# Kernel tuning notes

Measured on AMD Instinct MI355X. Metric: run time of the kernel, lower is better.

The kernel has to match this reference:

```python
import jax, jax.numpy as jnp
import numpy as np

RNN = 512        # rnn_units == embedding_units (required by LSTMCell input size)
ATT = 512        # attention_units
FEAT = 512       # feat_chans
VOCAB = 110
V1 = VOCAB + 1
MAX_LEN = 30
STEPS = MAX_LEN + 1
B, H, W = 32, 8, 32


def _lstm_cell(x, h, c, wih, whh, bih, bhh):
    # torch.nn.LSTMCell gate order: i, f, g, o
    gates = x @ wih.T + bih + h @ whh.T + bhh
    i, f, g, o = jnp.split(gates, 4, axis=-1)
    i, f, o = jax.nn.sigmoid(i), jax.nn.sigmoid(f), jax.nn.sigmoid(o)
    g = jnp.tanh(g)
    c_new = f * c + i * g
    h_new = o * jnp.tanh(c_new)
    return h_new, c_new


def setup_inputs() -> dict:
    key = jax.random.key(0)
    ks = jax.random.split(key, 16)
    s = 0.05

    def rn(k, shape):
        return jax.random.normal(k, shape, jnp.float32) * s

    return {
        "features": jax.random.normal(ks[0], (B, FEAT, H, W), jnp.float32),
        "holistic": jax.random.normal(ks[1], (B, RNN), jnp.float32),  # unused by forward (matches torch)
        "gt": jax.random.randint(ks[2], (B, STEPS), 0, V1),
        # AttentionModule params
        "W_feat": rn(ks[3], (ATT, FEAT, 3, 3)),
        "b_feat": jnp.zeros((ATT,), jnp.float32),
        "W_state": rn(ks[4], (ATT, RNN)),     # 1x1 conv, no bias
        "w_att": rn(ks[5], (ATT,)),           # 1x1 conv -> 1 channel, no bias
        # embedding (Linear, no bias): (embedding_units, vocab+1)
        "W_embed": rn(ks[6], (RNN, V1)),
        # LSTM cell 0
        "wih0": rn(ks[7], (4 * RNN, RNN)),
        "whh0": rn(ks[8], (4 * RNN, RNN)),
        "bih0": jnp.zeros((4 * RNN,), jnp.float32),
        "bhh0": jnp.zeros((4 * RNN,), jnp.float32),
        # LSTM cell 1
        "wih1": rn(ks[9], (4 * RNN, RNN)),
        "whh1": rn(ks[10], (4 * RNN, RNN)),
        "bih1": jnp.zeros((4 * RNN,), jnp.float32),
        "bhh1": jnp.zeros((4 * RNN,), jnp.float32),
        # output dense: (vocab+1, 2*rnn_units)
        "W_out": rn(ks[11], (V1, 2 * RNN)),
        "b_out": jnp.zeros((V1,), jnp.float32),
    }


def reference(features, holistic, gt, W_feat, b_feat, W_state, w_att, W_embed,
              wih0, whh0, bih0, bhh0, wih1, whh1, bih1, bhh1, W_out, b_out):
    Bsz, C, Hh, Ww = features.shape
    dt = features.dtype

    # feat_conv(features) is invariant across decode steps -> compute once
    feat_proj = jax.lax.conv_general_dilated(
        features, W_feat, window_strides=(1, 1), padding="SAME",
        dimension_numbers=("NCHW", "OIHW", "NCHW"),
    ) + b_feat[None, :, None, None]  # (B, ATT, H, W)

    # teacher-forced symbols: step 0 uses zeros, step t uses one_hot(gt[:, t-1])
    syms = jnp.concatenate(
        [jnp.zeros((Bsz, 1, V1), dt), jax.nn.one_hot(gt[:, :STEPS - 1], V1, dtype=dt)],
        axis=1,
    )
    syms = jnp.swapaxes(syms, 0, 1)  # (STEPS, B, V1)

    z = jnp.zeros((Bsz, RNN), dt)
    init = (z, z, z, z)  # h0, c0, h1, c1 (torch LSTMCell defaults to zero state)

    def step(carry, sym):
        h0, c0, h1, c1 = carry
        x = sym @ W_embed.T                                  # (B, RNN)
        h0, c0 = _lstm_cell(x, h0, c0, wih0, whh0, bih0, bhh0)
        h1, c1 = _lstm_cell(h0, h1, c1, wih1, whh1, bih1, bhh1)
        # attention glimpse: state is h1 broadcast as a 1x1 feature map
        sp = h1 @ W_state.T                                  # (B, ATT)
        proj = jnp.tanh(feat_proj + sp[:, :, None, None])    # (B, ATT, H, W)
        att = jnp.einsum("bahw,a->bhw", proj, w_att).reshape(Bsz, -1)
        att = jax.nn.softmax(att, axis=1).reshape(Bsz, Hh, Ww)
        glimpse = jnp.einsum("bchw,bhw->bc", features, att)  # (B, FEAT)
        logits = jnp.concatenate([h1, glimpse], axis=1) @ W_out.T + b_out
        return (h0, c0, h1, c1), logits

    _, logits = jax.lax.scan(step, init, syms)               # (STEPS, B, V1)
    return jnp.swapaxes(logits, 0, 1)                        # (B, STEPS, V1)
```

## Files before the change

### kernel.cpp

```cpp
#include <hip/hip_runtime.h>
#include <hip/hip_bf16.h>


#define RNN   512
#define V1    111
#define STEPS 31
#define HWP   256
#define POOLF 11008
#define NWG   128

typedef unsigned short ushortT;
typedef unsigned int   uintT;
typedef __attribute__((ext_vector_type(8))) short bf16x8;
typedef __attribute__((ext_vector_type(4))) float f32x4;

__device__ __forceinline__ float blo(uintT u){ union { uintT i; float f; } v; v.i = u << 16; return v.f; }
__device__ __forceinline__ float bhi(uintT u){ union { uintT i; float f; } v; v.i = u & 0xffff0000u; return v.f; }
__device__ __forceinline__ ushortT f2b(float f){
  __hip_bfloat16 h = __float2bfloat16(f);
  union { __hip_bfloat16 b; ushortT s; } v; v.b = h; return v.s;
}
__device__ __forceinline__ uintT packbf(float lo, float hi){
  return (uintT)f2b(lo) | ((uintT)f2b(hi) << 16);
}
__device__ __forceinline__ bf16x8 u4_to_b8(uint4 u){
  union { uint4 a; bf16x8 b; } v; v.a = u; return v.b;
}
__device__ __forceinline__ float sigf(float x){ return 1.f/(1.f + __expf(-x)); }
__device__ __forceinline__ float tanh_f(float x){ float e = __expf(2.f*x); return 1.f - 2.f/(e+1.f); }

__device__ __forceinline__ uintT sload_u(const uintT* p){
  return __hip_atomic_load((uintT*)p, __ATOMIC_RELAXED, __HIP_MEMORY_SCOPE_SYSTEM);
}
__device__ __forceinline__ void sstore_u(uintT* p, uintT v){
  __hip_atomic_store(p, v, __ATOMIC_RELAXED, __HIP_MEMORY_SCOPE_SYSTEM);
}

__global__ __launch_bounds__(256) void k_pre(const float* __restrict__ feat,
                                             const float* __restrict__ Wf,
                                             uintT* __restrict__ fT,
                                             uintT* __restrict__ wb){
  const int bid = blockIdx.x, tid = threadIdx.x;
  if (bid < 10880){
    int idx = bid*256 + tid;
    int cp = idx & 255;
    int r  = idx >> 8;
    int xi = r % 34;
    int q  = r / 34;
    int yy = q % 10;
    int b  = q / 10;
    float v0 = 0.f, v1 = 0.f;
    if (yy >= 1 && yy <= 8 && xi >= 1 && xi <= 32){
      size_t base = (((size_t)b*512 + 2*cp)*8 + (yy-1))*32 + (xi-1);
      v0 = feat[base];
      v1 = feat[base + 256];
    }
    fT[idx] = packbf(v0, v1);
  } else {
    int idx = (bid - 10880)*256 + tid;
    int cp = idx & 255;
    int r  = idx >> 8;
    int a  = r & 511;
    int t  = r >> 9;
    float v0 = Wf[((size_t)a*512 + 2*cp)*9 + t];
    float v1 = Wf[((size_t)a*512 + 2*cp + 1)*9 + t];
    wb[idx] = packbf(v0, v1);
  }
}

__global__ __launch_bounds__(256) void k_post(
    const float* __restrict__ w0, const float* __restrict__ w1,
    const float* __restrict__ w2, uintT* __restrict__ wgb,
    const float* __restrict__ Wst, uintT* __restrict__ WstTb,
    const float* __restrict__ Wout, uintT* __restrict__ Woutb,
    const float* __restrict__ wih0, const float* __restrict__ Wemb,
    const float* __restrict__ bih0, const float* __restrict__ bhh0,
    float* __restrict__ M0,
    float* __restrict__ st, uintT* __restrict__ h1hist, uintT* __restrict__ bar)
{
  const int bid = blockIdx.x, tid = threadIdx.x;
  if (bid < 6144){
    int idx = bid*256 + tid;
    int m = idx >> 19, r = idx & 524287;
    const float* s = (m==0)? w0 : (m==1)? w1 : w2;
    float2 v = *(const float2*)(s + 2*(size_t)r);
    wgb[idx] = packbf(v.x, v.y);
  } else if (bid < 6656){
    int idx = (bid-6144)*256 + tid;
    int u = idx >> 8, ap = idx & 255;
    WstTb[idx] = packbf(Wst[(size_t)(2*ap)*512 + u], Wst[(size_t)(2*ap+1)*512 + u]);
  } else if (bid < 6878){
    int idx = (bid-6656)*256 + tid;
    float2 v = *(const float2*)(Wout + 2*(size_t)idx);
    Woutb[idx] = packbf(v.x, v.y);
  } else if (bid < 7902){
    int j = (bid-6878)*2 + (tid >> 7);
    int g = tid & 127;
    float bs = bih0[j] + bhh0[j];
    if (g < V1){
      float acc = 0.f;
      const float* wr = wih0 + (size_t)j*512;
      for (int k=0;k<512;k++) acc += wr[k] * Wemb[(size_t)k*V1 + g];
      M0[(size_t)j*112 + g] = acc + bs;
    } else if (g == V1){
      M0[(size_t)j*112 + V1] = bs;
    }
  } else {
    int b2 = bid - 7902;
    if (b2 < 192)      st[b2*256 + tid] = 0.f;
    else if (b2 < 224) h1hist[(b2-192)*256 + tid] = 0u;
    else if (tid < 8)  bar[tid*32] = 0u;
  }
}

__global__ __launch_bounds__(256) void k_convm(const ushortT* __restrict__ fT,
                                               const ushortT* __restrict__ wb,
                                               const float* __restrict__ bfv,
                                               ushortT* __restrict__ fpj)
{
  __shared__ __align__(16) ushortT a_lds[136*72];
  __shared__ __align__(16) ushortT b_lds[256*72];
  const int tid = threadIdx.x;
  const int w   = tid >> 6;
  const int l   = tid & 63;
  const int kg  = l >> 4;
  const int ln  = l & 15;
  const int bid = blockIdx.x;
  const int nh  = bid & 1;
  const int mt  = bid >> 1;
  const int b   = mt >> 2;
  const int y0  = (mt & 3) * 2;
  const int a0  = nh * 256;

  f32x4 acc[4][4];
  #pragma unroll
  for (int nb=0; nb<4; nb++){
    float bv = bfv[a0 + w*64 + nb*16 + ln];
    #pragma unroll
    for (int mb=0; mb<4; mb++){
      acc[mb][nb][0]=bv; acc[mb][nb][1]=bv; acc[mb][nb][2]=bv; acc[mb][nb][3]=bv;
    }
  }

  const char* aSrc = (const char*)(fT + (((size_t)b*10 + y0)*34)*512);
  const char* wSrc = (const char*)wb;

  for (int c0 = 0; c0 < 512; c0 += 64){
    {
      const char* s = aSrc + (size_t)c0*2;
      #pragma unroll
      for (int i=0;i<4;i++){
        int idx = tid + i*256;
        int pos = idx >> 3, q = idx & 7;
        uint4 v = *(const uint4*)(s + (size_t)pos*1024 + q*16);
        *(uint4*)((char*)a_lds + pos*144 + q*16) = v;
      }
      if (tid < 64){
        int idx = 1024 + tid;
        int pos = idx >> 3, q = idx & 7;
        uint4 v = *(const uint4*)(s + (size_t)pos*1024 + q*16);
        *(uint4*)((char*)a_lds + pos*144 + q*16) = v;
      }
    }
    #pragma unroll
    for (int t=0; t<9; t++){
      const int ky = t/3, kx = t - (t/3)*3;
      {
        const char* s = wSrc + (((size_t)t*512 + a0)*512 + c0)*2;
        #pragma unroll
        for (int i=0;i<8;i++){
          int idx = tid + i*256;
          int ai = idx >> 3, q = idx & 7;
          uint4 v = *(const uint4*)(s + (size_t)ai*1024 + q*16);
          *(uint4*)((char*)b_lds + ai*144 + q*16) = v;
        }
      }
      __syncthreads();
      #pragma unroll
      for (int ks=0; ks<2; ks++){
        bf16x8 afr[4], bfr[4];
        #pragma unroll
        for (int mb=0; mb<4; mb++){
          int row = ((mb>>1) + ky)*34 + (mb&1)*16 + ln + kx;
          afr[mb] = *(const bf16x8*)((const char*)a_lds + row*144 + kg*16 + ks*64);
        }
        #pragma unroll
        for (int nb=0; nb<4; nb++){
          int ai = w*64 + nb*16 + ln;
          bfr[nb] = *(const bf16x8*)((const char*)b_lds + ai*144 + kg*16 + ks*64);
        }
        #pragma unroll
        for (int mb=0; mb<4; mb++)
          #pragma unroll
          for (int nb=0; nb<4; nb++)
            acc[mb][nb] = __builtin_amdgcn_mfma_f32_16x16x32_bf16(afr[mb], bfr[nb], acc[mb][nb], 0, 0, 0);
      }
      __syncthreads();
    }
  }

  #pragma unroll
  for (int mb=0; mb<4; mb++){
    #pragma unroll
    for (int nb=0; nb<4; nb++){
      int a = a0 + w*64 + nb*16 + ln;
      #pragma unroll
      for (int r4=0; r4<4; r4++){
        int pos = mb*16 + kg*4 + r4;
        fpj[((size_t)b*HWP + (y0*32 + pos))*512 + a] = f2b(acc[mb][nb][r4]);
      }
    }
  }
}

__device__ __forceinline__ void stage_state_s(uintT* __restrict__ hs,
                                              const uintT* __restrict__ src, int tid){
  #pragma unroll
  for (int i=0;i<16;i++){
    int g = tid + i*512;
    hs[(g >> 8)*268 + (g & 255)] = sload_u(&src[g]);
  }
}

__device__ __forceinline__ void sysbar(uintT* bar, int it, int bid){
  __syncthreads();
  if (threadIdx.x == 0){
    __hip_atomic_fetch_add(bar + (bid & 7)*32, 1u, __ATOMIC_RELAXED, __HIP_MEMORY_SCOPE_SYSTEM);
    const uintT tgt = (uintT)(it + 1) * (uintT)NWG;
    for (;;){
      uintT s = 0;
      #pragma unroll
      for (int i=0;i<8;i++)
        s += __hip_atomic_load(bar + i*32, __ATOMIC_RELAXED, __HIP_MEMORY_SCOPE_SYSTEM);
      if (s >= tgt) break;
      __builtin_amdgcn_s_sleep(8);
    }
  }
  __syncthreads();
}

__global__ __launch_bounds__(512) void k_rec(
    const int* __restrict__ gt, const float* __restrict__ M0,
    const uintT* __restrict__ wgb,
    const float* __restrict__ bih1, const float* __restrict__ bhh1,
    float* __restrict__ st, uintT* __restrict__ h1hist, uintT* __restrict__ bar)
{
  __shared__ __align__(16) float pool[POOLF];
  const int tid = threadIdx.x, bid = blockIdx.x;
  uintT* h0bf = (uintT*)st;
  float* c0T  = st + 16384;
  float* c1T  = st + 32768;

  const bool isA = bid < 64;
  const int w   = tid >> 6;
  const int l   = tid & 63;
  const int kg  = l >> 4;
  const int ln  = l & 15;
  const int ks2 = w >> 2;
  const int rt  = (w >> 1) & 1;
  const int nh  = w & 1;
  const int u0  = (isA ? bid : bid - 64) * 8;
  const int jrow = (ln >> 2)*512 + u0 + rt*4 + (ln & 3);

  uint4 wA[8], wB1[8], wB2[8];
  if (isA){
    const uintT* wp = wgb + (size_t)jrow*256 + kg*4;
    #pragma unroll
    for (int s8=0; s8<8; s8++) wA[s8] = *(const uint4*)(wp + (ks2*8 + s8)*16);
  } else {
    const uintT* wp1 = wgb + 524288  + (size_t)jrow*256 + kg*4;
    const uintT* wp2 = wgb + 1048576 + (size_t)jrow*256 + kg*4;
    #pragma unroll
    for (int s8=0; s8<8; s8++){
      wB1[s8] = *(const uint4*)(wp1 + (ks2*8 + s8)*16);
      wB2[s8] = *(const uint4*)(wp2 + (ks2*8 + s8)*16);
    }
  }

  uintT* hs = (uintT*)pool;
  float* gs = pool + 8576;
  float* hv = pool + 10688;
  const ushortT* hb = (const ushortT*)hs + (nh*16 + ln)*536 + kg*8;

  for (int L = 0; L <= STEPS; L++){
    const int t = isA ? L : L - 1;
    if ((isA && t <= STEPS-1) || (!isA && t >= 0)){
      f32x4 acc = {0.f, 0.f, 0.f, 0.f};
      if (isA){
        stage_state_s(hs, h0bf + ((t+1)&1)*8192, tid);
        __syncthreads();
        #pragma unroll
        for (int s8=0; s8<8; s8++){
          int s = ks2*8 + s8;
          bf16x8 bfr = *(const bf16x8*)(hb + s*32);
          acc = __builtin_amdgcn_mfma_f32_16x16x32_bf16(u4_to_b8(wA[s8]), bfr, acc, 0, 0, 0);
        }
      } else {
        stage_state_s(hs, h0bf + (t&1)*8192, tid);
        __syncthreads();
        #pragma unroll
        for (int s8=0; s8<8; s8++){
          int s = ks2*8 + s8;
          bf16x8 bfr = *(const bf16x8*)(hb + s*32);
          acc = __builtin_amdgcn_mfma_f32_16x16x32_bf16(u4_to_b8(wB1[s8]), bfr, acc, 0, 0, 0);
        }
        __syncthreads();
        stage_state_s(hs, h1hist + (size_t)t*8192, tid);
        __syncthreads();
        #pragma unroll
        for (int s8=0; s8<8; s8++){
          int s = ks2*8 + s8;
          bf16x8 bfr = *(const bf16x8*)(hb + s*32);
          acc = __builtin_amdgcn_mfma_f32_16x16x32_bf16(u4_to_b8(wB2[s8]), bfr, acc, 0, 0, 0);
        }
      }
      #pragma unroll
      for (int r=0;r<4;r++)
        gs[(ks2*32 + kg*8 + rt*4 + r)*33 + nh*16 + ln] = acc[r];
      __syncthreads();

      if (tid < 256){
        const int ul = tid >> 5, b = tid & 31, u = u0 + ul;
        float g4[4];
        #pragma unroll
        for (int g=0; g<4; g++){
          float sacc = gs[(g*8+ul)*33 + b] + gs[(32 + g*8+ul)*33 + b];
          int j = g*512 + u;
          if (isA){
            int sym = (t > 0) ? gt[b*STEPS + t - 1] : V1;
            sacc += M0[(size_t)j*112 + sym];
          } else {
            sacc += bih1[j] + bhh1[j];
          }
          g4[g] = sacc;
        }
        float* cT = isA ? c0T : c1T;
        int idx = u*32 + b;
        float cn = sigf(g4[1])*cT[idx] + sigf(g4[0])*tanh_f(g4[2]);
        cT[idx] = cn;
        float h = sigf(g4[3])*tanh_f(cn);
        hv[ul*33 + b] = h;
      }
      __syncthreads();
      if (tid < 128){
        const int up = tid >> 5, b = tid & 31;
        uintT v = packbf(hv[(up*2)*33 + b], hv[(up*2+1)*33 + b]);
        if (isA) sstore_u(&h0bf[(t&1)*8192 + b*256 + (u0>>1) + up], v);
        else     sstore_u(&h1hist[(size_t)(t+1)*8192 + b*256 + (u0>>1) + up], v);
      }
    }
    if (L < STEPS) sysbar(bar, L, bid);
  }
}

__global__ __launch_bounds__(512) void k_att(
    const float* __restrict__ features, const uintT* __restrict__ h1hist,
    const ushortT* __restrict__ fpj, const uintT* __restrict__ WstTb,
    const float* __restrict__ watt, const uintT* __restrict__ Woutb,
    const float* __restrict__ bout, float* __restrict__ out)
{
  __shared__ __align__(16) float pool[7488];
  const int tid = threadIdx.x;
  const int b = blockIdx.x / STEPS, r = blockIdx.x % STEPS;
  float* h1s   = pool;
  float* spsl  = pool + 512;
  float* watts = pool + 1024;
  float* pals  = pool + 1536;
  float* attw  = pool + 2048;
  float* glim  = pool + 2304;
  float* red   = pool + 2816;
  float* opart = pool + 2880;
  float* sppt  = pool + 3392;

  if (tid < 256){
    uintT hvw = h1hist[(size_t)(r+1)*8192 + b*256 + tid];
    h1s[2*tid]   = blo(hvw);
    h1s[2*tid+1] = bhi(hvw);
  }
  watts[tid] = watt[tid];
  __syncthreads();

  {
    int ap4 = tid & 63, uq = tid >> 6;
    float a8[8] = {0.f,0.f,0.f,0.f,0.f,0.f,0.f,0.f};
    const uint4* wp = (const uint4*)(WstTb + (size_t)(uq*64)*256) + ap4;
    const float* hq = h1s + uq*64;
    #pragma unroll 8
    for (int u=0; u<64; u++){
      uint4 q = wp[(size_t)u*64];
      float h = hq[u];
      a8[0] += blo(q.x)*h; a8[1] += bhi(q.x)*h;
      a8[2] += blo(q.y)*h; a8[3] += bhi(q.y)*h;
      a8[4] += blo(q.z)*h; a8[5] += bhi(q.z)*h;
      a8[6] += blo(q.w)*h; a8[7] += bhi(q.w)*h;
    }
    #pragma unroll
    for (int j=0;j<8;j++) sppt[uq*512 + ap4*8 + j] = a8[j];
  }
  __syncthreads();
  {
    float s = 0.f;
    #pragma unroll
    for (int uq=0;uq<8;uq++) s += sppt[uq*512 + tid];
    spsl[tid] = s;
  }
  __syncthreads();

  {
    int p = tid & 255, ac = tid >> 8;
    const uint4* fr = (const uint4*)(fpj + ((size_t)b*HWP + p)*512 + ac*256);
    float al2 = 0.f;
    #pragma unroll 8
    for (int kb=0;kb<32;kb++){
      uint4 q = fr[kb];
      float v[8] = {blo(q.x),bhi(q.x),blo(q.y),bhi(q.y),blo(q.z),bhi(q.z),blo(q.w),bhi(q.w)};
      int a0 = ac*256 + kb*8;
      #pragma unroll
      for (int i=0;i<8;i++)
        al2 += watts[a0+i] * tanh_f(v[i] + spsl[a0+i]);
    }
    pals[tid] = al2;
  }
  __syncthreads();
  {
    float al2 = (tid < 256) ? (pals[tid] + pals[256+tid]) : -1e30f;
    float m = al2;
    #pragma unroll
    for (int off=32; off>0; off>>=1) m = fmaxf(m, __shfl_xor(m, off));
    if (tid < 256 && (tid & 63)==0) red[tid>>6] = m;
    __syncthreads();
    m = fmaxf(fmaxf(red[0],red[1]), fmaxf(red[2],red[3]));
    float e = (tid < 256) ? __expf(al2 - m) : 0.f;
    float s = e;
    #pragma unroll
    for (int off=32; off>0; off>>=1) s += __shfl_xor(s, off);
    __syncthreads();
    if (tid < 256 && (tid & 63)==0) red[tid>>6] = s;
    __syncthreads();
    if (tid < 256){
      float sa = red[0]+red[1]+red[2]+red[3];
      attw[tid] = e / sa;
    }
  }
  __syncthreads();
  {
    const float4* fr = (const float4*)(features + ((size_t)b*512 + tid)*256);
    float acc = 0.f;
    #pragma unroll 8
    for (int kb=0;kb<64;kb++){
      float4 v = fr[kb];
      const float* aw = attw + kb*4;
      acc += v.x*aw[0] + v.y*aw[1] + v.z*aw[2] + v.w*aw[3];
    }
    glim[tid] = acc;
  }
  __syncthreads();
  {
    int q = tid >> 7, o = tid & 127;
    float acc = 0.f;
    if (o < V1){
      const uint4* wr4 = (const uint4*)(Woutb + (size_t)o*512 + q*128);
      const float* src = (q < 2) ? (h1s + q*256) : (glim + (q-2)*256);
      #pragma unroll 8
      for (int kb=0;kb<32;kb++){
        uint4 w4 = wr4[kb];
        const float* sx = src + kb*8;
        acc += blo(w4.x)*sx[0] + bhi(w4.x)*sx[1] + blo(w4.y)*sx[2] + bhi(w4.y)*sx[3]
             + blo(w4.z)*sx[4] + bhi(w4.z)*sx[5] + blo(w4.w)*sx[6] + bhi(w4.w)*sx[7];
      }
    }
    opart[tid] = acc;
  }
  __syncthreads();
  if (tid < V1){
    float acc = bout[tid] + opart[tid] + opart[128+tid] + opart[256+tid] + opart[384+tid];
    out[(size_t)b*STEPS*V1 + (size_t)r*V1 + tid] = acc;
  }
}

extern "C" void kernel_launch(void* const* d_in, const int* in_sizes, int n_in,
                              void* d_out, int out_size, void* d_ws, size_t ws_size,
                              hipStream_t stream)
{
  const float* features = (const float*)d_in[0];
  const int*   gt       = (const int*)d_in[2];
  const float* Wf    = (const float*)d_in[3];
  const float* bfv   = (const float*)d_in[4];
  const float* Wst   = (const float*)d_in[5];
  const float* watt  = (const float*)d_in[6];
  const float* Wemb  = (const float*)d_in[7];
  const float* wih0  = (const float*)d_in[8];
  const float* whh0  = (const float*)d_in[9];
  const float* bih0  = (const float*)d_in[10];
  const float* bhh0  = (const float*)d_in[11];
  const float* wih1  = (const float*)d_in[12];
  const float* whh1  = (const float*)d_in[13];
  const float* bih1  = (const float*)d_in[14];
  const float* bhh1  = (const float*)d_in[15];
  const float* Wout  = (const float*)d_in[16];
  const float* bout  = (const float*)d_in[17];
  float* out = (float*)d_out;

  char* wsb = (char*)d_ws;
  ushortT* fpj    = (ushortT*)(wsb + 0);
  uintT*   h1hist = (uintT*)  (wsb + 8388608);
  float*   M0     = (float*)  (wsb + 16777216);
  uintT*   wgb    = (uintT*)  (wsb + 17694720);
  uintT*   Woutb  = (uintT*)  (wsb + 23986176);
  uintT*   bar    = (uintT*)  (wsb + 24213504);
  uintT*   WstTb  = (uintT*)  (wsb + 24215552);
  float*   st     = (float*)  (wsb + 24739840);
  uintT*   fTt    = (uintT*)  (wsb + 8388608);
  ushortT* wbt    = (ushortT*)(wsb + 19529728);

  k_pre  <<<15488, 256, 0, stream>>>(features, Wf, fTt, (uintT*)wbt);
  k_convm<<<256,   256, 0, stream>>>((const ushortT*)fTt, wbt, bfv, fpj);
  k_post <<<8127,  256, 0, stream>>>(whh0, wih1, whh1, wgb,
                                     Wst, WstTb, Wout, Woutb,
                                     wih0, Wemb, bih0, bhh0, M0,
                                     st, h1hist, bar);
  k_rec  <<<NWG,   512, 0, stream>>>(gt, M0, wgb, bih1, bhh1, st, h1hist, bar);
  k_att  <<<32*STEPS, 512, 0, stream>>>(features, h1hist, fpj, WstTb, watt,
                                        Woutb, bout, out);
  (void)in_sizes; (void)n_in; (void)out_size; (void)ws_size;
}
```

Baseline: 756.7 us.

## Fuse attention into persistent recurrence kernel with dedicated per-batch attention workgroups

After: 1.806 ms. 2.39x slower.

```diff
diff --git a/kernel.cpp b/kernel.cpp
--- a/kernel.cpp
+++ b/kernel.cpp
@@ -7,7 +7,7 @@
 #define STEPS 31
 #define HWP   256
 #define POOLF 11008
-#define NWG   128
+#define NWG   160
 
 typedef unsigned short ushortT;
 typedef unsigned int   uintT;
@@ -98,10 +98,15 @@
     int g = tid & 127;
     float bs = bih0[j] + bhh0[j];
     if (g < V1){
-      float acc = 0.f;
+      float a0=0.f, a1=0.f, a2=0.f, a3=0.f;
       const float* wr = wih0 + (size_t)j*512;
-      for (int k=0;k<512;k++) acc += wr[k] * Wemb[(size_t)k*V1 + g];
-      M0[(size_t)j*112 + g] = acc + bs;
+      for (int k=0;k<512;k+=4){
+        a0 += wr[k]   * Wemb[(size_t)k*V1 + g];
+        a1 += wr[k+1] * Wemb[(size_t)(k+1)*V1 + g];
+        a2 += wr[k+2] * Wemb[(size_t)(k+2)*V1 + g];
+        a3 += wr[k+3] * Wemb[(size_t)(k+3)*V1 + g];
+      }
+      M0[(size_t)j*112 + g] = ((a0+a1)+(a2+a3)) + bs;
     } else if (g == V1){
       M0[(size_t)j*112 + V1] = bs;
     }
@@ -239,11 +244,15 @@
   __syncthreads();
 }
 
-__global__ __launch_bounds__(512) void k_rec(
+__global__ __launch_bounds__(512) void k_main(
     const int* __restrict__ gt, const float* __restrict__ M0,
     const uintT* __restrict__ wgb,
     const float* __restrict__ bih1, const float* __restrict__ bhh1,
-    float* __restrict__ st, uintT* __restrict__ h1hist, uintT* __restrict__ bar)
+    float* __restrict__ st, uintT* __restrict__ h1hist, uintT* __restrict__ bar,
+    const float* __restrict__ features, const ushortT* __restrict__ fpj,
+    const uintT* __restrict__ WstTb, const float* __restrict__ watt,
+    const uintT* __restrict__ Woutb, const float* __restrict__ bout,
+    float* __restrict__ out)
 {
   __shared__ __align__(16) float pool[POOLF];
   const int tid = threadIdx.x, bid = blockIdx.x;
@@ -251,7 +260,9 @@
   float* c0T  = st + 16384;
   float* c1T  = st + 32768;
 
-  const bool isA = bid < 64;
+  const bool isGate = bid < 128;
+  const bool isA    = bid < 64;
+
   const int w   = tid >> 6;
   const int l   = tid & 63;
   const int kg  = l >> 4;
@@ -263,18 +274,22 @@
   const int jrow = (ln >> 2)*512 + u0 + rt*4 + (ln & 3);
 
   uint4 wA[8], wB1[8], wB2[8];
-  if (isA){
-    const uintT* wp = wgb + (size_t)jrow*256 + kg*4;
-    #pragma unroll
-    for (int s8=0; s8<8; s8++) wA[s8] = *(const uint4*)(wp + (ks2*8 + s8)*16);
+  if (isGate){
+    if (isA){
+      const uintT* wp = wgb + (size_t)jrow*256 + kg*4;
+      #pragma unroll
+      for (int s8=0; s8<8; s8++) wA[s8] = *(const uint4*)(wp + (ks2*8 + s8)*16);
+    } else {
+      const uintT* wp1 = wgb + 524288  + (size_t)jrow*256 + kg*4;
+      const uintT* wp2 = wgb + 1048576 + (size_t)jrow*256 + kg*4;
+      #pragma unroll
+      for (int s8=0; s8<8; s8++){
+        wB1[s8] = *(const uint4*)(wp1 + (ks2*8 + s8)*16);
+        wB2[s8] = *(const uint4*)(wp2 + (ks2*8 + s8)*16);
+      }
+    }
   } else {
-    const uintT* wp1 = wgb + 524288  + (size_t)jrow*256 + kg*4;
-    const uintT* wp2 = wgb + 1048576 + (size_t)jrow*256 + kg*4;
-    #pragma unroll
-    for (int s8=0; s8<8; s8++){
-      wB1[s8] = *(const uint4*)(wp1 + (ks2*8 + s8)*16);
-      wB2[s8] = *(const uint4*)(wp2 + (ks2*8 + s8)*16);
-    }
+    pool[1024 + tid] = watt[tid];
   }
 
   uintT* hs = (uintT*)pool;
@@ -282,199 +297,194 @@
   float* hv = pool + 10688;
   const ushortT* hb = (const ushortT*)hs + (nh*16 + ln)*536 + kg*8;
 
-  for (int L = 0; L <= STEPS; L++){
-    const int t = isA ? L : L - 1;
-    if ((isA && t <= STEPS-1) || (!isA && t >= 0)){
-      f32x4 acc = {0.f, 0.f, 0.f, 0.f};
-      if (isA){
-        stage_state_s(hs, h0bf + ((t+1)&1)*8192, tid);
-        __syncthreads();
+  for (int L = 0; L <= STEPS + 1; L++){
+    if (isGate){
+      const int t = isA ? L : L - 1;
+      if (t >= 0 && t <= STEPS-1){
+        f32x4 acc = {0.f, 0.f, 0.f, 0.f};
+        if (isA){
+          stage_state_s(hs, h0bf + ((t+1)&1)*8192, tid);
+          __syncthreads();
+          #pragma unroll
+          for (int s8=0; s8<8; s8++){
+            int s = ks2*8 + s8;
+            bf16x8 bfr = *(const bf16x8*)(hb + s*32);
+            acc = __builtin_amdgcn_mfma_f32_16x16x32_bf16(u4_to_b8(wA[s8]), bfr, acc, 0, 0, 0);
+          }
+        } else {
+          stage_state_s(hs, h0bf + (t&1)*8192, tid);
+          __syncthreads();
+          #pragma unroll
+          for (int s8=0; s8<8; s8++){
+            int s = ks2*8 + s8;
+            bf16x8 bfr = *(const bf16x8*)(hb + s*32);
+            acc = __builtin_amdgcn_mfma_f32_16x16x32_bf16(u4_to_b8(wB1[s8]), bfr, acc, 0, 0, 0);
+          }
+          __syncthreads();
+          stage_state_s(hs, h1hist + (size_t)t*8192, tid);
+          __syncthreads();
+          #pragma unroll
+          for (int s8=0; s8<8; s8++){
+            int s = ks2*8 + s8;
+            bf16x8 bfr = *(const bf16x8*)(hb + s*32);
+            acc = __builtin_amdgcn_mfma_f32_16x16x32_bf16(u4_to_b8(wB2[s8]), bfr, acc, 0, 0, 0);
+          }
+        }
         #pragma unroll
-        for (int s8=0; s8<8; s8++){
-          int s = ks2*8 + s8;
-          bf16x8 bfr = *(const bf16x8*)(hb + s*32);
-          acc = __builtin_amdgcn_mfma_f32_16x16x32_bf16(u4_to_b8(wA[s8]), bfr, acc, 0, 0, 0);
-        }
-      } else {
-        stage_state_s(hs, h0bf + (t&1)*8192, tid);
-        __syncthreads();
-        #pragma unroll
-        for (int s8=0; s8<8; s8++){
-          int s = ks2*8 + s8;
-          bf16x8 bfr = *(const bf16x8*)(hb + s*32);
-          acc = __builtin_amdgcn_mfma_f32_16x16x32_bf16(u4_to_b8(wB1[s8]), bfr, acc, 0, 0, 0);
-        }
-        __syncthreads();
-        stage_state_s(hs, h1hist + (size_t)t*8192, tid);
-        __syncthreads();
-        #pragma unroll
-        for (int s8=0; s8<8; s8++){
-          int s = ks2*8 + s8;
-          bf16x8 bfr = *(const bf16x8*)(hb + s*32);
-          acc = __builtin_amdgcn_mfma_f32_16x16x32_bf16(u4_to_b8(wB2[s8]), bfr, acc, 0, 0, 0);
-        }
-      }
-      #pragma unroll
-      for (int r=0;r<4;r++)
-        gs[(ks2*32 + kg*8 + rt*4 + r)*33 + nh*16 + ln] = acc[r];
-      __syncthreads();
-
-      if (tid < 256){
-        const int ul = tid >> 5, b = tid & 31, u = u0 + ul;
-        float g4[4];
-        #pragma unroll
-        for (int g=0; g<4; g++){
-          float sacc = gs[(g*8+ul)*33 + b] + gs[(32 + g*8+ul)*33 + b];
-          int j = g*512 + u;
-          if (isA){
-            int sym = (t > 0) ? gt[b*STEPS + t - 1] : V1;
-            sacc += M0[(size_t)j*112 + sym];
-          } else {
-            sacc += bih1[j] + bhh1[j];
-          }
-          g4[g] = sacc;
-        }
-        float* cT = isA ? c0T : c1T;
-        int idx = u*32 + b;
-        float cn = sigf(g4[1])*cT[idx] + sigf(g4[0])*tanh_f(g4[2]);
-        cT[idx] = cn;
-        float h = sigf(g4[3])*tanh_f(cn);
-        hv[ul*33 + b] = h;
-      }
-      __syncthreads();
-      if (tid < 128){
-        const int up = tid >> 5, b = tid & 31;
-        uintT v = packbf(hv[(up*2)*33 + b], hv[(up*2+1)*33 + b]);
-        if (isA) sstore_u(&h0bf[(t&1)*8192 + b*256 + (u0>>1) + up], v);
-        else     sstore_u(&h1hist[(size_t)(t+1)*8192 + b*256 + (u0>>1) + up], v);
-      }
-    }
-    if (L < STEPS) sysbar(bar, L, bid);
-  }
-}
-
-__global__ __launch_bounds__(512) void k_att(
-    const float* __restrict__ features, const uintT* __restrict__ h1hist,
-    const ushortT* __restrict__ fpj, const uintT* __restrict__ WstTb,
-    const float* __restrict__ watt, const uintT* __restrict__ Woutb,
-    const float* __restrict__ bout, float* __restrict__ out)
-{
-  __shared__ __align__(16) float pool[7488];
-  const int tid = threadIdx.x;
-  const int b = blockIdx.x / STEPS, r = blockIdx.x % STEPS;
-  float* h1s   = pool;
-  float* spsl  = pool + 512;
-  float* watts = pool + 1024;
-  float* pals  = pool + 1536;
-  float* attw  = pool + 2048;
-  float* glim  = pool + 2304;
-  float* red   = pool + 2816;
-  float* opart = pool + 2880;
-  float* sppt  = pool + 3392;
-
-  if (tid < 256){
-    uintT hvw = h1hist[(size_t)(r+1)*8192 + b*256 + tid];
-    h1s[2*tid]   = blo(hvw);
-    h1s[2*tid+1] = bhi(hvw);
-  }
-  watts[tid] = watt[tid];
-  __syncthreads();
-
-  {
-    int ap4 = tid & 63, uq = tid >> 6;
-    float a8[8] = {0.f,0.f,0.f,0.f,0.f,0.f,0.f,0.f};
-    const uint4* wp = (const uint4*)(WstTb + (size_t)(uq*64)*256) + ap4;
-    const float* hq = h1s + uq*64;
-    #pragma unroll 8
-    for (int u=0; u<64; u++){
-      uint4 q = wp[(size_t)u*64];
-      float h = hq[u];
-      a8[0] += blo(q.x)*h; a8[1] += bhi(q.x)*h;
-      a8[2] += blo(q.y)*h; a8[3] += bhi(q.y)*h;
-      a8[4] += blo(q.z)*h; a8[5] += bhi(q.z)*h;
-      a8[6] += blo(q.w)*h; a8[7] += bhi(q.w)*h;
-    }
-    #pragma unroll
-    for (int j=0;j<8;j++) sppt[uq*512 + ap4*8 + j] = a8[j];
-  }
-  __syncthreads();
-  {
-    float s = 0.f;
-    #pragma unroll
-    for (int uq=0;uq<8;uq++) s += sppt[uq*512 + tid];
-    spsl[tid] = s;
-  }
-  __syncthreads();
-
-  {
-    int p = tid & 255, ac = tid >> 8;
-    const uint4* fr = (const uint4*)(fpj + ((size_t)b*HWP + p)*512 + ac*256);
-    float al2 = 0.f;
-    #pragma unroll 8
-    for (int kb=0;kb<32;kb++){
-      uint4 q = fr[kb];
-      float v[8] = {blo(q.x),bhi(q.x),blo(q.y),bhi(q.y),blo(q.z),bhi(q.z),blo(q.w),bhi(q.w)};
-      int a0 = ac*256 + kb*8;
-      #pragma unroll
-      for (int i=0;i<8;i++)
-        al2 += watts[a0+i] * tanh_f(v[i] + spsl[a0+i]);
-    }
-    pals[tid] = al2;
-  }
-  __syncthreads();
-  {
-    float al2 = (tid < 256) ? (pals[tid] + pals[256+tid]) : -1e30f;
-    float m = al2;
-    #pragma unroll
-    for (int off=32; off>0; off>>=1) m = fmaxf(m, __shfl_xor(m, off));
-    if (tid < 256 && (tid & 63)==0) red[tid>>6] = m;
-    __syncthreads();
-    m = fmaxf(fmaxf(red[0],red[1]), fmaxf(red[2],red[3]));
-    float e = (tid < 256) ? __expf(al2 - m) : 0.f;
-    float s = e;
-    #pragma unroll
-    for (int off=32; off>0; off>>=1) s += __shfl_xor(s, off);
-    __syncthreads();
-    if (tid < 256 && (tid & 63)==0) red[tid>>6] = s;
-    __syncthreads();
-    if (tid < 256){
-      float sa = red[0]+red[1]+red[2]+red[3];
-      attw[tid] = e / sa;
-    }
-  }
-  __syncthreads();
-  {
-    const float4* fr = (const float4*)(features + ((size_t)b*512 + tid)*256);
-    float acc = 0.f;
-    #pragma unroll 8
-    for (int kb=0;kb<64;kb++){
-      float4 v = fr[kb];
-      const float* aw = attw + kb*4;
-      acc += v.x*aw[0] + v.y*aw[1] + v.z*aw[2] + v.w*aw[3];
-    }
-    glim[tid] = acc;
-  }
-  __syncthreads();
-  {
-    int q = tid >> 7, o = tid & 127;
-    float acc = 0.f;
-    if (o < V1){
-      const uint4* wr4 = (const uint4*)(Woutb + (size_t)o*512 + q*128);
-      const float* src = (q < 2) ? (h1s + q*256) : (glim + (q-2)*256);
-      #pragma unroll 8
-      for (int kb=0;kb<32;kb++){
-        uint4 w4 = wr4[kb];
-        const float* sx = src + kb*8;
-        acc += blo(w4.x)*sx[0] + bhi(w4.x)*sx[1] + blo(w4.y)*sx[2] + bhi(w4.y)*sx[3]
-             + blo(w4.z)*sx[4] + bhi(w4.z)*sx[5] + blo(w4.w)*sx[6] + bhi(w4.w)*sx[7];
-      }
-    }
-    opart[tid] = acc;
-  }
-  __syncthreads();
-  if (tid < V1){
-    float acc = bout[tid] + opart[tid] + opart[128+tid] + opart[256+tid] + opart[384+tid];
-    out[(size_t)b*STEPS*V1 + (size_t)r*V1 + tid] = acc;
+        for (int r=0;r<4;r++)
+          gs[(ks2*32 + kg*8 + rt*4 + r)*33 + nh*16 + ln] = acc[r];
+        __syncthreads();
+
+        if (tid < 256){
+          const int ul = tid >> 5, b = tid & 31, u = u0 + ul;
+          float g4[4];
+          #pragma unroll
+          for (int g=0; g<4; g++){
+            float sacc = gs[(g*8+ul)*33 + b] + gs[(32 + g*8+ul)*33 + b];
+            int j = g*512 + u;
+            if (isA){
+              int sym = (t > 0) ? gt[b*STEPS + t - 1] : V1;
+              sacc += M0[(size_t)j*112 + sym];
+            } else {
+              sacc += bih1[j] + bhh1[j];
+            }
+            g4[g] = sacc;
+          }
+          float* cT = isA ? c0T : c1T;
+          int idx = u*32 + b;
+          float cn = sigf(g4[1])*cT[idx] + sigf(g4[0])*tanh_f(g4[2]);
+          cT[idx] = cn;
+          float h = sigf(g4[3])*tanh_f(cn);
+          hv[ul*33 + b] = h;
+        }
+        __syncthreads();
+        if (tid < 128){
+          const int up = tid >> 5, b = tid & 31;
+          uintT v = packbf(hv[(up*2)*33 + b], hv[(up*2+1)*33 + b]);
+          if (isA) sstore_u(&h0bf[(t&1)*8192 + b*256 + (u0>>1) + up], v);
+          else     sstore_u(&h1hist[(size_t)(t+1)*8192 + b*256 + (u0>>1) + up], v);
+        }
+      }
+    } else {
+      const int rs = L - 2;
+      if (rs >= 0 && rs <= STEPS-1){
+        const int b = bid - 128;
+        float* h1s   = pool;
+        float* spsl  = pool + 512;
+        float* watts = pool + 1024;
+        float* pals  = pool + 1536;
+        float* attw  = pool + 2048;
+        float* glim  = pool + 2304;
+        float* red   = pool + 2816;
+        float* opart = pool + 2880;
+        float* sppt  = pool + 3392;
+
+        if (tid < 256){
+          uintT hvw = sload_u(&h1hist[(size_t)(rs+1)*8192 + b*256 + tid]);
+          h1s[2*tid]   = blo(hvw);
+          h1s[2*tid+1] = bhi(hvw);
+        }
+        __syncthreads();
+
+        {
+          int ap4 = tid & 63, uq = tid >> 6;
+          float a8[8] = {0.f,0.f,0.f,0.f,0.f,0.f,0.f,0.f};
+          const uint4* wp = (const uint4*)(WstTb + (size_t)(uq*64)*256) + ap4;
+          const float* hq = h1s + uq*64;
+          #pragma unroll 8
+          for (int u=0; u<64; u++){
+            uint4 q = wp[(size_t)u*64];
+            float h = hq[u];
+            a8[0] += blo(q.x)*h; a8[1] += bhi(q.x)*h;
+            a8[2] += blo(q.y)*h; a8[3] += bhi(q.y)*h;
+            a8[4] += blo(q.z)*h; a8[5] += bhi(q.z)*h;
+            a8[6] += blo(q.w)*h; a8[7] += bhi(q.w)*h;
+          }
+          #pragma unroll
+          for (int j=0;j<8;j++) sppt[uq*512 + ap4*8 + j] = a8[j];
+        }
+        __syncthreads();
+        {
+          float s = 0.f;
+          #pragma unroll
+          for (int uq=0;uq<8;uq++) s += sppt[uq*512 + tid];
+          spsl[tid] = s;
+        }
+        __syncthreads();
+
+        {
+          int p = tid & 255, ac = tid >> 8;
+          const uint4* fr = (const uint4*)(fpj + ((size_t)b*HWP + p)*512 + ac*256);
+          float al2 = 0.f;
+          #pragma unroll 8
+          for (int kb=0;kb<32;kb++){
+            uint4 q = fr[kb];
+            float v[8] = {blo(q.x),bhi(q.x),blo(q.y),bhi(q.y),blo(q.z),bhi(q.z),blo(q.w),bhi(q.w)};
+            int a0 = ac*256 + kb*8;
+            #pragma unroll
+            for (int i=0;i<8;i++)
+              al2 += watts[a0+i] * tanh_f(v[i] + spsl[a0+i]);
+          }
+          pals[tid] = al2;
+        }
+        __syncthreads();
+        {
+          float al2 = (tid < 256) ? (pals[tid] + pals[256+tid]) : -1e30f;
+          float m = al2;
+          #pragma unroll
+          for (int off=32; off>0; off>>=1) m = fmaxf(m, __shfl_xor(m, off));
+          if (tid < 256 && (tid & 63)==0) red[tid>>6] = m;
+          __syncthreads();
+          m = fmaxf(fmaxf(red[0],red[1]), fmaxf(red[2],red[3]));
+          float e = (tid < 256) ? __expf(al2 - m) : 0.f;
+          float s = e;
+          #pragma unroll
+          for (int off=32; off>0; off>>=1) s += __shfl_xor(s, off);
+          __syncthreads();
+          if (tid < 256 && (tid & 63)==0) red[tid>>6] = s;
+          __syncthreads();
+          if (tid < 256){
+            float sa = red[0]+red[1]+red[2]+red[3];
+            attw[tid] = e / sa;
+          }
+        }
+        __syncthreads();
+        {
+          const float4* fr = (const float4*)(features + ((size_t)b*512 + tid)*256);
+          float acc = 0.f;
+          #pragma unroll 8
+          for (int kb=0;kb<64;kb++){
+            float4 v = fr[kb];
+            const float* aw = attw + kb*4;
+            acc += v.x*aw[0] + v.y*aw[1] + v.z*aw[2] + v.w*aw[3];
+          }
+          glim[tid] = acc;
+        }
+        __syncthreads();
+        {
+          int q = tid >> 7, o = tid & 127;
+          float acc = 0.f;
+          if (o < V1){
+            const uint4* wr4 = (const uint4*)(Woutb + (size_t)o*512 + q*128);
+            const float* src = (q < 2) ? (h1s + q*256) : (glim + (q-2)*256);
+            #pragma unroll 8
+            for (int kb=0;kb<32;kb++){
+              uint4 w4 = wr4[kb];
+              const float* sx = src + kb*8;
+              acc += blo(w4.x)*sx[0] + bhi(w4.x)*sx[1] + blo(w4.y)*sx[2] + bhi(w4.y)*sx[3]
+                   + blo(w4.z)*sx[4] + bhi(w4.z)*sx[5] + blo(w4.w)*sx[6] + bhi(w4.w)*sx[7];
+            }
+          }
+          opart[tid] = acc;
+        }
+        __syncthreads();
+        if (tid < V1){
+          float acc = bout[tid] + opart[tid] + opart[128+tid] + opart[256+tid] + opart[384+tid];
+          out[(size_t)b*STEPS*V1 + (size_t)rs*V1 + tid] = acc;
+        }
+      }
+    }
+    if (L <= STEPS) sysbar(bar, L, bid);
   }
 }
 
@@ -519,8 +529,7 @@
                                      Wst, WstTb, Wout, Woutb,
                                      wih0, Wemb, bih0, bhh0, M0,
                                      st, h1hist, bar);
-  k_rec  <<<NWG,   512, 0, stream>>>(gt, M0, wgb, bih1, bhh1, st, h1hist, bar);
-  k_att  <<<32*STEPS, 512, 0, stream>>>(features, h1hist, fpj, WstTb, watt,
-                                        Woutb, bout, out);
+  k_main <<<NWG,   512, 0, stream>>>(gt, M0, wgb, bih1, bhh1, st, h1hist, bar,
+                                     features, fpj, WstTb, watt, Woutb, bout, out);
   (void)in_sizes; (void)n_in; (void)out_size; (void)ws_size;
 }
```

## Replace global grid barrier with per-step producer-consumer flags between LSTM layers

Applied to the files above, without the earlier changes.

Measured after the change: 673.7 us. 11.0% less time.

```diff
diff --git a/kernel.cpp b/kernel.cpp
--- a/kernel.cpp
+++ b/kernel.cpp
@@ -6,7 +6,6 @@
 #define V1    111
 #define STEPS 31
 #define HWP   256
-#define POOLF 11008
 #define NWG   128
 
 typedef unsigned short ushortT;
@@ -34,6 +33,12 @@
 }
 __device__ __forceinline__ void sstore_u(uintT* p, uintT v){
   __hip_atomic_store(p, v, __ATOMIC_RELAXED, __HIP_MEMORY_SCOPE_SYSTEM);
+}
+__device__ __forceinline__ void wait_ge(uintT* p, uintT tgt){
+  for (;;){
+    if (__hip_atomic_load(p, __ATOMIC_RELAXED, __HIP_MEMORY_SCOPE_SYSTEM) >= tgt) break;
+    __builtin_amdgcn_s_sleep(2);
+  }
 }
 
 __global__ __launch_bounds__(256) void k_pre(const float* __restrict__ feat,
@@ -76,7 +81,8 @@
     const float* __restrict__ wih0, const float* __restrict__ Wemb,
     const float* __restrict__ bih0, const float* __restrict__ bhh0,
     float* __restrict__ M0,
-    float* __restrict__ st, uintT* __restrict__ h1hist, uintT* __restrict__ bar)
+    float* __restrict__ st, uintT* __restrict__ h1hist,
+    uintT* __restrict__ h0hist, uintT* __restrict__ bar)
 {
   const int bid = blockIdx.x, tid = threadIdx.x;
   if (bid < 6144){
@@ -98,18 +104,24 @@
     int g = tid & 127;
     float bs = bih0[j] + bhh0[j];
     if (g < V1){
-      float acc = 0.f;
+      float a0=0.f, a1=0.f, a2=0.f, a3=0.f;
       const float* wr = wih0 + (size_t)j*512;
-      for (int k=0;k<512;k++) acc += wr[k] * Wemb[(size_t)k*V1 + g];
-      M0[(size_t)j*112 + g] = acc + bs;
+      for (int k=0;k<512;k+=4){
+        a0 += wr[k]   * Wemb[(size_t)k*V1 + g];
+        a1 += wr[k+1] * Wemb[(size_t)(k+1)*V1 + g];
+        a2 += wr[k+2] * Wemb[(size_t)(k+2)*V1 + g];
+        a3 += wr[k+3] * Wemb[(size_t)(k+3)*V1 + g];
+      }
+      M0[(size_t)j*112 + g] = ((a0+a1)+(a2+a3)) + bs;
     } else if (g == V1){
       M0[(size_t)j*112 + V1] = bs;
     }
   } else {
     int b2 = bid - 7902;
-    if (b2 < 192)      st[b2*256 + tid] = 0.f;
-    else if (b2 < 224) h1hist[(b2-192)*256 + tid] = 0u;
-    else if (tid < 8)  bar[tid*32] = 0u;
+    if (b2 < 128)      st[b2*256 + tid] = 0.f;
+    else if (b2 < 160) h1hist[(b2-128)*256 + tid] = 0u;
+    else if (b2 < 192) h0hist[(b2-160)*256 + tid] = 0u;
+    else               bar[(b2-192)*256 + tid] = 0u;
   }
 }
 
@@ -222,34 +234,19 @@
   }
 }
 
-__device__ __forceinline__ void sysbar(uintT* bar, int it, int bid){
-  __syncthreads();
-  if (threadIdx.x == 0){
-    __hip_atomic_fetch_add(bar + (bid & 7)*32, 1u, __ATOMIC_RELAXED, __HIP_MEMORY_SCOPE_SYSTEM);
-    const uintT tgt = (uintT)(it + 1) * (uintT)NWG;
-    for (;;){
-      uintT s = 0;
-      #pragma unroll
-      for (int i=0;i<8;i++)
-        s += __hip_atomic_load(bar + i*32, __ATOMIC_RELAXED, __HIP_MEMORY_SCOPE_SYSTEM);
-      if (s >= tgt) break;
-      __builtin_amdgcn_s_sleep(8);
-    }
-  }
-  __syncthreads();
-}
-
 __global__ __launch_bounds__(512) void k_rec(
     const int* __restrict__ gt, const float* __restrict__ M0,
     const uintT* __restrict__ wgb,
     const float* __restrict__ bih1, const float* __restrict__ bhh1,
-    float* __restrict__ st, uintT* __restrict__ h1hist, uintT* __restrict__ bar)
+    float* __restrict__ st, uintT* __restrict__ h1hist,
+    uintT* __restrict__ h0hist, uintT* __restrict__ bar)
 {
-  __shared__ __align__(16) float pool[POOLF];
+  __shared__ __align__(16) float pool[19584];
   const int tid = threadIdx.x, bid = blockIdx.x;
-  uintT* h0bf = (uintT*)st;
-  float* c0T  = st + 16384;
-  float* c1T  = st + 32768;
+  float* c0T = st;
+  float* c1T = st + 16384;
+  uintT* arrA = bar;
+  uintT* arrB = bar + 1024;
 
   const bool isA = bid < 64;
   const int w   = tid >> 6;
@@ -262,63 +259,43 @@
   const int u0  = (isA ? bid : bid - 64) * 8;
   const int jrow = (ln >> 2)*512 + u0 + rt*4 + (ln & 3);
 
-  uint4 wA[8], wB1[8], wB2[8];
+  uintT* hs0 = (uintT*)pool;
+  uintT* hs1 = (uintT*)pool + 8576;
+  float* gs  = pool + 17152;
+  float* hv  = pool + 19264;
+  const ushortT* hb0 = (const ushortT*)hs0 + (nh*16 + ln)*536 + kg*8;
+  const ushortT* hb1 = (const ushortT*)hs1 + (nh*16 + ln)*536 + kg*8;
+
+  uint4 wA[8], wB[16];
   if (isA){
     const uintT* wp = wgb + (size_t)jrow*256 + kg*4;
     #pragma unroll
     for (int s8=0; s8<8; s8++) wA[s8] = *(const uint4*)(wp + (ks2*8 + s8)*16);
   } else {
-    const uintT* wp1 = wgb + 524288  + (size_t)jrow*256 + kg*4;
-    const uintT* wp2 = wgb + 1048576 + (size_t)jrow*256 + kg*4;
-    #pragma unroll
-    for (int s8=0; s8<8; s8++){
-      wB1[s8] = *(const uint4*)(wp1 + (ks2*8 + s8)*16);
-      wB2[s8] = *(const uint4*)(wp2 + (ks2*8 + s8)*16);
-    }
-  }
-
-  uintT* hs = (uintT*)pool;
-  float* gs = pool + 8576;
-  float* hv = pool + 10688;
-  const ushortT* hb = (const ushortT*)hs + (nh*16 + ln)*536 + kg*8;
-
-  for (int L = 0; L <= STEPS; L++){
-    const int t = isA ? L : L - 1;
-    if ((isA && t <= STEPS-1) || (!isA && t >= 0)){
+    const uintT* wp = wgb + (ks2 ? 1048576 : 524288) + (size_t)jrow*256 + kg*4;
+    #pragma unroll
+    for (int s=0; s<16; s++) wB[s] = *(const uint4*)(wp + s*16);
+  }
+
+  for (int t = 0; t <= STEPS-1; t++){
+    if (isA){
+      if (t > 0){
+        if (tid == 0) wait_ge(arrA + (t-1)*32, 64u);
+        __syncthreads();
+      }
+      stage_state_s(hs0, h0hist + (size_t)t*8192, tid);
+      __syncthreads();
       f32x4 acc = {0.f, 0.f, 0.f, 0.f};
-      if (isA){
-        stage_state_s(hs, h0bf + ((t+1)&1)*8192, tid);
-        __syncthreads();
-        #pragma unroll
-        for (int s8=0; s8<8; s8++){
-          int s = ks2*8 + s8;
-          bf16x8 bfr = *(const bf16x8*)(hb + s*32);
-          acc = __builtin_amdgcn_mfma_f32_16x16x32_bf16(u4_to_b8(wA[s8]), bfr, acc, 0, 0, 0);
-        }
-      } else {
-        stage_state_s(hs, h0bf + (t&1)*8192, tid);
-        __syncthreads();
-        #pragma unroll
-        for (int s8=0; s8<8; s8++){
-          int s = ks2*8 + s8;
-          bf16x8 bfr = *(const bf16x8*)(hb + s*32);
-          acc = __builtin_amdgcn_mfma_f32_16x16x32_bf16(u4_to_b8(wB1[s8]), bfr, acc, 0, 0, 0);
-        }
-        __syncthreads();
-        stage_state_s(hs, h1hist + (size_t)t*8192, tid);
-        __syncthreads();
-        #pragma unroll
-        for (int s8=0; s8<8; s8++){
-          int s = ks2*8 + s8;
-          bf16x8 bfr = *(const bf16x8*)(hb + s*32);
-          acc = __builtin_amdgcn_mfma_f32_16x16x32_bf16(u4_to_b8(wB2[s8]), bfr, acc, 0, 0, 0);
-        }
+      #pragma unroll
+      for (int s8=0; s8<8; s8++){
+        int s = ks2*8 + s8;
+        bf16x8 bfr = *(const bf16x8*)(hb0 + s*32);
+        acc = __builtin_amdgcn_mfma_f32_16x16x32_bf16(u4_to_b8(wA[s8]), bfr, acc, 0, 0, 0);
       }
       #pragma unroll
       for (int r=0;r<4;r++)
         gs[(ks2*32 + kg*8 + rt*4 + r)*33 + nh*16 + ln] = acc[r];
       __syncthreads();
-
       if (tid < 256){
         const int ul = tid >> 5, b = tid & 31, u = u0 + ul;
         float g4[4];
@@ -326,30 +303,67 @@
         for (int g=0; g<4; g++){
           float sacc = gs[(g*8+ul)*33 + b] + gs[(32 + g*8+ul)*33 + b];
           int j = g*512 + u;
-          if (isA){
-            int sym = (t > 0) ? gt[b*STEPS + t - 1] : V1;
-            sacc += M0[(size_t)j*112 + sym];
-          } else {
-            sacc += bih1[j] + bhh1[j];
-          }
-          g4[g] = sacc;
+          int sym = (t > 0) ? gt[b*STEPS + t - 1] : V1;
+          g4[g] = sacc + M0[(size_t)j*112 + sym];
         }
-        float* cT = isA ? c0T : c1T;
         int idx = u*32 + b;
-        float cn = sigf(g4[1])*cT[idx] + sigf(g4[0])*tanh_f(g4[2]);
-        cT[idx] = cn;
-        float h = sigf(g4[3])*tanh_f(cn);
-        hv[ul*33 + b] = h;
+        float cn = sigf(g4[1])*c0T[idx] + sigf(g4[0])*tanh_f(g4[2]);
+        c0T[idx] = cn;
+        hv[ul*33 + b] = sigf(g4[3])*tanh_f(cn);
       }
       __syncthreads();
       if (tid < 128){
         const int up = tid >> 5, b = tid & 31;
-        uintT v = packbf(hv[(up*2)*33 + b], hv[(up*2+1)*33 + b]);
-        if (isA) sstore_u(&h0bf[(t&1)*8192 + b*256 + (u0>>1) + up], v);
-        else     sstore_u(&h1hist[(size_t)(t+1)*8192 + b*256 + (u0>>1) + up], v);
-      }
-    }
-    if (L < STEPS) sysbar(bar, L, bid);
+        sstore_u(&h0hist[(size_t)(t+1)*8192 + b*256 + (u0>>1) + up],
+                 packbf(hv[(up*2)*33 + b], hv[(up*2+1)*33 + b]));
+      }
+      __syncthreads();
+      if (tid == 0)
+        __hip_atomic_fetch_add(arrA + t*32, 1u, __ATOMIC_RELAXED, __HIP_MEMORY_SCOPE_SYSTEM);
+    } else {
+      if (tid == 0){
+        wait_ge(arrA + t*32, 64u);
+        if (t > 0) wait_ge(arrB + (t-1)*32, 64u);
+      }
+      __syncthreads();
+      stage_state_s(hs0, h0hist + (size_t)(t+1)*8192, tid);
+      stage_state_s(hs1, h1hist + (size_t)t*8192, tid);
+      __syncthreads();
+      f32x4 acc = {0.f, 0.f, 0.f, 0.f};
+      const ushortT* hbm = ks2 ? hb1 : hb0;
+      #pragma unroll
+      for (int s=0; s<16; s++){
+        bf16x8 bfr = *(const bf16x8*)(hbm + s*32);
+        acc = __builtin_amdgcn_mfma_f32_16x16x32_bf16(u4_to_b8(wB[s]), bfr, acc, 0, 0, 0);
+      }
+      #pragma unroll
+      for (int r=0;r<4;r++)
+        gs[(ks2*32 + kg*8 + rt*4 + r)*33 + nh*16 + ln] = acc[r];
+      __syncthreads();
+      if (tid < 256){
+        const int ul = tid >> 5, b = tid & 31, u = u0 + ul;
+        float g4[4];
+        #pragma unroll
+        for (int g=0; g<4; g++){
+          float sacc = gs[(g*8+ul)*33 + b] + gs[(32 + g*8+ul)*33 + b];
+          int j = g*512 + u;
+          g4[g] = sacc + bih1[j] + bhh1[j];
+        }
+        int idx = u*32 + b;
+        float cn = sigf(g4[1])*c1T[idx] + sigf(g4[0])*tanh_f(g4[2]);
+        c1T[idx] = cn;
+        hv[ul*33 + b] = sigf(g4[3])*tanh_f(cn);
+      }
+      __syncthreads();
+      if (tid < 128){
+        const int up = tid >> 5, b = tid & 31;
+        sstore_u(&h1hist[(size_t)(t+1)*8192 + b*256 + (u0>>1) + up],
+                 packbf(hv[(up*2)*33 + b], hv[(up*2+1)*33 + b]));
+      }
+      __syncthreads();
+      if (tid == 0)
+        __hip_atomic_fetch_add(arrB + t*32, 1u, __ATOMIC_RELAXED, __HIP_MEMORY_SCOPE_SYSTEM);
+    }
   }
 }
 
@@ -504,22 +518,24 @@
   char* wsb = (char*)d_ws;
   ushortT* fpj    = (ushortT*)(wsb + 0);
   uintT*   h1hist = (uintT*)  (wsb + 8388608);
+  uintT*   h0hist = (uintT*)  (wsb + 9437184);
   float*   M0     = (float*)  (wsb + 16777216);
   uintT*   wgb    = (uintT*)  (wsb + 17694720);
   uintT*   Woutb  = (uintT*)  (wsb + 23986176);
-  uintT*   bar    = (uintT*)  (wsb + 24213504);
   uintT*   WstTb  = (uintT*)  (wsb + 24215552);
   float*   st     = (float*)  (wsb + 24739840);
+  uintT*   bar    = (uintT*)  (wsb + 24936448);
   uintT*   fTt    = (uintT*)  (wsb + 8388608);
   ushortT* wbt    = (ushortT*)(wsb + 19529728);
 
   k_pre  <<<15488, 256, 0, stream>>>(features, Wf, fTt, (uintT*)wbt);
   k_convm<<<256,   256, 0, stream>>>((const ushortT*)fTt, wbt, bfv, fpj);
-  k_post <<<8127,  256, 0, stream>>>(whh0, wih1, whh1, wgb,
+  k_post <<<8102,  256, 0, stream>>>(whh0, wih1, whh1, wgb,
                                      Wst, WstTb, Wout, Woutb,
                                      wih0, Wemb, bih0, bhh0, M0,
-                                     st, h1hist, bar);
-  k_rec  <<<NWG,   512, 0, stream>>>(gt, M0, wgb, bih1, bhh1, st, h1hist, bar);
+                                     st, h1hist, h0hist, bar);
+  k_rec  <<<NWG,   512, 0, stream>>>(gt, M0, wgb, bih1, bhh1, st,
+                                     h1hist, h0hist, bar);
   k_att  <<<32*STEPS, 512, 0, stream>>>(features, h1hist, fpj, WstTb, watt,
                                         Woutb, bout, out);
   (void)in_sizes; (void)n_in; (void)out_size; (void)ws_size;
```
